# Performance work log

Measured on AMD Instinct MI355X. Metric: run time of the kernel, lower is better.

## Reference

```python
import jax, jax.numpy as jnp
import numpy as np

B, N, FD, HD, G = 32, 512, 768, 384, 3
ALPHA = 0.2  # LeakyReLU slope
NEG = -9e15


def layer_norm(x, g, b, eps=1e-5):
    m = jnp.mean(x, axis=-1, keepdims=True)
    v = jnp.var(x, axis=-1, keepdims=True)
    return (x - m) / jnp.sqrt(v + eps) * g + b


def gat_layer(x, adj, W, a):
    # x: [B,N,FD], adj: [N,N], W: [FD,HD], a: [2*HD]
    h = jnp.einsum('bnf,fd->bnd', x, W)  # [B,N,HD]
    # concat score decomposes: e_ij = lrelu(h_i . a[:HD] + h_j . a[HD:])
    e1 = h @ a[:HD]   # [B,N]
    e2 = h @ a[HD:]   # [B,N]
    e = jax.nn.leaky_relu(e1[:, :, None] + e2[:, None, :], ALPHA)  # [B,N,N]
    e = jnp.where(adj[None] > 0, e, NEG)
    att = jax.nn.softmax(e, axis=2)  # masked softmax over neighbors
    h_prime = jnp.einsum('bij,bjd->bid', att, h)
    return jax.nn.elu(h_prime)  # concat=True -> ELU


def setup_inputs() -> dict:
    key = jax.random.key(0)
    ks = jax.random.split(key, 10)
    s = 0.05
    return {
        'x': jax.random.normal(ks[0], (B, N, FD), jnp.float32),
        'adj': jax.random.randint(ks[1], (G, N, N), 0, 2),
        'W': jax.random.normal(ks[2], (G, FD, HD), jnp.float32) * s,
        'a': jax.random.normal(ks[3], (G, 2 * HD), jnp.float32) * s,
        'log_unc': jnp.zeros((G,), jnp.float32),
        'gate_w': jax.random.normal(ks[4], (FD, G), jnp.float32) * s,
        'gate_b': jnp.zeros((G,), jnp.float32),
        'ln1_g': jnp.ones((HD,), jnp.float32),
        'ln1_b': jnp.zeros((HD,), jnp.float32),
        'w1': jax.random.normal(ks[5], (HD, HD), jnp.float32) * s,
        'b1': jnp.zeros((HD,), jnp.float32),
        'w2': jax.random.normal(ks[6], (HD, FD), jnp.float32) * s,
        'b2': jnp.zeros((FD,), jnp.float32),
        'ln2_g': jnp.ones((FD,), jnp.float32),
        'ln2_b': jnp.zeros((FD,), jnp.float32),
    }


def reference(x, adj, W, a, log_unc, gate_w, gate_b, ln1_g, ln1_b,
              w1, b1, w2, b2, ln2_g, ln2_b):
    # global (uncertainty) weights
    unc = jnp.exp(log_unc)
    attw = jax.nn.softmax(1.0 / (unc + 1e-8))  # [G]
    # content gates from batch-averaged features
    avg = jnp.mean(x, axis=0)                          # [N,FD]
    cg = jax.nn.softmax(avg @ gate_w + gate_b, axis=-1)  # [N,G]
    # per-graph GAT + LayerNorm, vmapped over the G graphs
    gouts = jax.vmap(lambda ad, Wi, ai: layer_norm(gat_layer(x, ad, Wi, ai), ln1_g, ln1_b))(adj, W, a)  # [G,B,N,HD]
    weights = 0.7 * attw[:, None, None, None] + 0.3 * cg.T[:, None, :, None]  # [G,1|B,N,1]
    fused = jnp.sum(weights * gouts, axis=0)  # [B,N,HD]
    # output projection + LayerNorm
    proj = jax.nn.relu(fused @ w1 + b1) @ w2 + b2
    proj = layer_norm(proj, ln2_g, ln2_b)
    # residual gate
    gv = jax.nn.sigmoid(jnp.sum(proj * x, axis=-1, keepdims=True) / np.sqrt(FD).astype(np.float32))
    return gv * x + (1.0 - gv) * proj
```

## Files before the change

kernel.cpp:

```cpp
#include <hip/hip_runtime.h>

typedef unsigned short ushort_t;
typedef unsigned int uint_t;
typedef __bf16 bf16x8 __attribute__((ext_vector_type(8)));
typedef float f32x4 __attribute__((ext_vector_type(4)));
typedef unsigned int u32x4 __attribute__((ext_vector_type(4)));
typedef unsigned short u16x4 __attribute__((ext_vector_type(4)));
typedef unsigned short u16x8 __attribute__((ext_vector_type(8)));

#define B_SZ 32
#define N_SZ 512
#define FD_SZ 768
#define HD_SZ 384
#define G_SZ 3
#define M_SZ (B_SZ * N_SZ)
#define ALPHA_LR 0.2f
#define NEGV -9.0e15f
#define VTILE (HD_SZ * 32)
#define PSLICE ((size_t)M_SZ * HD_SZ)

__device__ __forceinline__ float bf2f(ushort_t u) { return __uint_as_float(((uint_t)u) << 16); }
__device__ __forceinline__ ushort_t f2bf(float f) {
  uint_t x = __float_as_uint(f);
  return (ushort_t)((x + 0x7fffu + ((x >> 16) & 1u)) >> 16);
}

__device__ __forceinline__ void gload_lds16(const ushort_t* g, ushort_t* l) {
  __builtin_amdgcn_global_load_lds(
      (const __attribute__((address_space(1))) uint_t*)(const void*)g,
      (__attribute__((address_space(3))) uint_t*)(void*)l, 16, 0, 0);
}

__global__ __launch_bounds__(256) void transpose_f2b(
    const float* __restrict__ src, ushort_t* __restrict__ dst, int R, int C) {
  size_t total = (size_t)R * C;
  size_t base = (size_t)blockIdx.z * total;
  size_t i = (size_t)blockIdx.x * 256 + threadIdx.x;
  if (i < total) {
    int r = (int)(i / C), c = (int)(i % C);
    dst[base + (size_t)c * R + r] = f2bf(src[base + i]);
  }
}

__global__ __launch_bounds__(256) void cast_f2b(
    const float* __restrict__ src, ushort_t* __restrict__ dst) {
  size_t i = (size_t)blockIdx.x * 256 + threadIdx.x;
  f32x4 v = ((const f32x4*)src)[i];
  u16x4 p;
  p[0] = f2bf(v.x); p[1] = f2bf(v.y); p[2] = f2bf(v.z); p[3] = f2bf(v.w);
  ((u16x4*)dst)[i] = p;
}

__global__ __launch_bounds__(256) void pack_adj(
    const int* __restrict__ adj, uint_t* __restrict__ am) {
  size_t i = (size_t)blockIdx.x * 256 + threadIdx.x;
  unsigned long long mask = __ballot(adj[i] != 0);
  int lane = threadIdx.x & 63;
  if ((lane & 31) == 0) am[i >> 5] = (uint_t)(mask >> (lane & 32));
}

__global__ __launch_bounds__(256) void gate_kernel(
    const float* __restrict__ x, const float* __restrict__ gate_w,
    const float* __restrict__ gate_b, float* __restrict__ cg) {
  int n = blockIdx.x;
  int tid = threadIdx.x;
  float a0 = 0.f, a1 = 0.f, a2 = 0.f;
  for (int f = tid; f < FD_SZ; f += 256) {
    float s = 0.f;
#pragma unroll
    for (int b = 0; b < B_SZ; b++) s += x[((size_t)b * N_SZ + n) * FD_SZ + f];
    float avg = s * (1.0f / B_SZ);
    a0 += avg * gate_w[f * 3 + 0];
    a1 += avg * gate_w[f * 3 + 1];
    a2 += avg * gate_w[f * 3 + 2];
  }
  for (int m = 1; m < 64; m <<= 1) {
    a0 += __shfl_xor(a0, m, 64);
    a1 += __shfl_xor(a1, m, 64);
    a2 += __shfl_xor(a2, m, 64);
  }
  __shared__ float red[3][4];
  int wave = tid >> 6, lane = tid & 63;
  if (lane == 0) { red[0][wave] = a0; red[1][wave] = a1; red[2][wave] = a2; }
  __syncthreads();
  if (tid == 0) {
    float l0 = red[0][0] + red[0][1] + red[0][2] + red[0][3] + gate_b[0];
    float l1 = red[1][0] + red[1][1] + red[1][2] + red[1][3] + gate_b[1];
    float l2 = red[2][0] + red[2][1] + red[2][2] + red[2][3] + gate_b[2];
    float mx = fmaxf(l0, fmaxf(l1, l2));
    float e0 = __expf(l0 - mx), e1 = __expf(l1 - mx), e2 = __expf(l2 - mx);
    float inv = 1.0f / (e0 + e1 + e2);
    cg[n * 3 + 0] = e0 * inv;
    cg[n * 3 + 1] = e1 * inv;
    cg[n * 3 + 2] = e2 * inv;
  }
}

template <bool RELU, bool OUTBF16, bool HASBIAS, bool VFOUT>
__global__ __launch_bounds__(256) void gemm_kernel(
    const ushort_t* __restrict__ Ab, size_t strideA,
    const ushort_t* __restrict__ Bt, size_t strideB,
    const float* __restrict__ bias,
    void* __restrict__ Cv, size_t strideC,
    int M, int K, int Nc) {
  __shared__ __attribute__((aligned(16))) ushort_t As[128 * 32];
  __shared__ __attribute__((aligned(16))) ushort_t Bs[128 * 32];
  int tid = threadIdx.x, wave = tid >> 6, lane = tid & 63;
  int m0 = blockIdx.y * 128, n0 = blockIdx.x * 128;
  const ushort_t* A = Ab + (size_t)blockIdx.z * strideA;
  const ushort_t* Bb = Bt + (size_t)blockIdx.z * strideB;

  f32x4 acc[4][4];
  f32x4 z4 = {0.f, 0.f, 0.f, 0.f};
#pragma unroll
  for (int i = 0; i < 4; i++)
#pragma unroll
    for (int j = 0; j < 4; j++) acc[i][j] = z4;

  int wm = (wave & 1) * 64, wn = (wave >> 1) * 64;
  int srow = lane >> 2, schk = (lane & 3) * 8;

  for (int kt = 0; kt < K; kt += 32) {
    __syncthreads();
#pragma unroll
    for (int i = 0; i < 2; i++) {
      int rowBase = wave * 32 + i * 16;
      gload_lds16(A + (size_t)(m0 + rowBase + srow) * K + kt + schk,
                  As + rowBase * 32);
      gload_lds16(Bb + (size_t)(n0 + rowBase + srow) * K + kt + schk,
                  Bs + rowBase * 32);
    }
    __syncthreads();
    bf16x8 af[4], bfr[4];
#pragma unroll
    for (int t = 0; t < 4; t++) {
      af[t] = *(const bf16x8*)(As + (wm + t * 16 + (lane & 15)) * 32 + (lane >> 4) * 8);
      bfr[t] = *(const bf16x8*)(Bs + (wn + t * 16 + (lane & 15)) * 32 + (lane >> 4) * 8);
    }
#pragma unroll
    for (int mt = 0; mt < 4; mt++)
#pragma unroll
      for (int nt = 0; nt < 4; nt++)
        acc[mt][nt] = __builtin_amdgcn_mfma_f32_16x16x32_bf16(af[mt], bfr[nt], acc[mt][nt], 0, 0, 0);
  }

  if (VFOUT) {
#pragma unroll
    for (int mt = 0; mt < 4; mt++) {
#pragma unroll
      for (int nt = 0; nt < 4; nt++) {
        int d = n0 + wn + nt * 16 + (lane & 15);
        int gm = m0 + wm + mt * 16 + (lane >> 4) * 4;
        int b = gm >> 9, jt = (gm >> 5) & 15, j2 = gm & 31;
        u16x4 pk;
#pragma unroll
        for (int r2 = 0; r2 < 4; r2++) pk[r2] = f2bf(acc[mt][nt][r2]);
        size_t off = ((size_t)((blockIdx.z * B_SZ + b) * 16 + jt)) * VTILE + (size_t)d * 32 + j2;
        *(u16x4*)((ushort_t*)Cv + off) = pk;
      }
    }
  } else {
#pragma unroll
    for (int mt = 0; mt < 4; mt++) {
#pragma unroll
      for (int nt = 0; nt < 4; nt++) {
        int gn = n0 + wn + nt * 16 + (lane & 15);
        float bvs = HASBIAS ? bias[gn] : 0.f;
#pragma unroll
        for (int r2 = 0; r2 < 4; r2++) {
          int gm = m0 + wm + mt * 16 + (lane >> 4) * 4 + r2;
          float v = acc[mt][nt][r2] + bvs;
          if (RELU) v = v > 0.f ? v : 0.f;
          size_t off = (size_t)blockIdx.z * strideC + (size_t)gm * Nc + gn;
          if (OUTBF16) ((ushort_t*)Cv)[off] = f2bf(v);
          else ((float*)Cv)[off] = v;
        }
      }
    }
  }
}

__global__ __launch_bounds__(256) void e12_kernel(
    const ushort_t* __restrict__ vf, const float* __restrict__ a,
    float* __restrict__ e1, float* __restrict__ e2) {
  __shared__ float a1s[HD_SZ], a2s[HD_SZ];
  int g = blockIdx.y;
  int tid = threadIdx.x;
  for (int i = tid; i < HD_SZ; i += 256) {
    a1s[i] = a[g * 2 * HD_SZ + i];
    a2s[i] = a[g * 2 * HD_SZ + HD_SZ + i];
  }
  __syncthreads();
  int m = blockIdx.x * 64 + (tid >> 2), dq = tid & 3;
  int b = m >> 9, jt = (m >> 5) & 15, j2 = m & 31;
  const ushort_t* col = vf + ((size_t)((g * B_SZ + b) * 16 + jt)) * VTILE + j2;
  float s1 = 0.f, s2 = 0.f;
#pragma unroll 4
  for (int k = 0; k < 96; k++) {
    int d = dq * 96 + k;
    float h = bf2f(col[d * 32]);
    s1 += h * a1s[d];
    s2 += h * a2s[d];
  }
  s1 += __shfl_xor(s1, 1, 64); s1 += __shfl_xor(s1, 2, 64);
  s2 += __shfl_xor(s2, 1, 64); s2 += __shfl_xor(s2, 2, 64);
  if (dq == 0) {
    e1[(size_t)g * M_SZ + m] = s1;
    e2[(size_t)g * M_SZ + m] = s2;
  }
}

__global__ __launch_bounds__(512, 4) void attn_kernel(
    const uint_t* __restrict__ adjm, const ushort_t* __restrict__ vf,
    const float* __restrict__ e1, const float* __restrict__ e2,
    const float* __restrict__ cg, const float* __restrict__ log_unc,
    const float* __restrict__ ln1g, const float* __restrict__ ln1b,
    ushort_t* __restrict__ pf) {
  __shared__ __attribute__((aligned(16))) ushort_t Pb[32][520];
  __shared__ float e2s[512];
  __shared__ float e1r[32];
  __shared__ uint_t amS[32][16];
  __shared__ float lng[HD_SZ], lnb[HD_SZ];
  __shared__ float cgr[32];
  __shared__ float s1s[32][8], s2s[32][8];

  int tid = threadIdx.x, wave = tid >> 6, lane = tid & 63;
  int quad = lane >> 4, l15 = lane & 15;
  int g = blockIdx.z;
  int L = blockIdx.x + (blockIdx.y << 4);
  int b = (L & 7) + ((L >> 7) << 3);
  int i0 = ((L >> 3) & 15) * 32;

  float iv0 = 1.f / (__expf(log_unc[0]) + 1e-8f);
  float iv1 = 1.f / (__expf(log_unc[1]) + 1e-8f);
  float iv2 = 1.f / (__expf(log_unc[2]) + 1e-8f);
  float mxa = fmaxf(iv0, fmaxf(iv1, iv2));
  float w0 = __expf(iv0 - mxa), w1 = __expf(iv1 - mxa), w2 = __expf(iv2 - mxa);
  float wsum = 1.f / (w0 + w1 + w2);
  float attwg = (g == 0 ? w0 : (g == 1 ? w1 : w2)) * wsum;

  if (tid < HD_SZ) {
    lng[tid] = ln1g[tid];
    lnb[tid] = ln1b[tid];
  }
  if (tid < 32) {
    cgr[tid] = cg[(i0 + tid) * 3 + g];
    e1r[tid] = e1[((size_t)g * B_SZ + b) * N_SZ + i0 + tid];
  }
  amS[tid >> 4][tid & 15] = adjm[((size_t)g * N_SZ + i0 + (tid >> 4)) * 16 + (tid & 15)];
  e2s[tid] = e2[((size_t)g * B_SZ + b) * N_SZ + tid];
  __syncthreads();

#pragma unroll
  for (int rr = 0; rr < 4; rr++) {
    int rw = wave * 4 + rr;
    float e1v = e1r[rw];
    float sv[8];
    float m = -3.0e38f;
#pragma unroll
    for (int jj = 0; jj < 8; jj++) {
      int j = lane + jj * 64;
      float s = e1v + e2s[j];
      s = s > 0.f ? s : ALPHA_LR * s;
      uint_t mw = amS[rw][(lane >> 5) + jj * 2];
      s = ((mw >> (j & 31)) & 1u) ? s : NEGV;
      sv[jj] = s;
      m = fmaxf(m, s);
    }
    for (int msk = 1; msk < 64; msk <<= 1) m = fmaxf(m, __shfl_xor(m, msk, 64));
    float sum = 0.f;
#pragma unroll
    for (int jj = 0; jj < 8; jj++) {
      float e = __expf(sv[jj] - m);
      sv[jj] = e;
      sum += e;
    }
    for (int msk = 1; msk < 64; msk <<= 1) sum += __shfl_xor(sum, msk, 64);
    float inv = 1.0f / sum;
#pragma unroll
    for (int jj = 0; jj < 8; jj++) Pb[rw][lane + jj * 64] = f2bf(sv[jj] * inv);
  }
  __syncthreads();

  f32x4 acc[2][3];
  f32x4 z4 = {0.f, 0.f, 0.f, 0.f};
#pragma unroll
  for (int mt = 0; mt < 2; mt++)
#pragma unroll
    for (int t = 0; t < 3; t++) acc[mt][t] = z4;
  const ushort_t* vbase = vf + ((size_t)(g * B_SZ + b) * 16) * VTILE;
  __builtin_amdgcn_s_setprio(1);
#pragma unroll 2
  for (int j0 = 0; j0 < N_SZ; j0 += 32) {
    const ushort_t* vtile = vbase + (size_t)(j0 >> 5) * VTILE;
    bf16x8 af0 = *(const bf16x8*)(&Pb[l15][j0 + quad * 8]);
    bf16x8 af1 = *(const bf16x8*)(&Pb[16 + l15][j0 + quad * 8]);
#pragma unroll
    for (int t = 0; t < 3; t++) {
      bf16x8 bf = *(const bf16x8*)(vtile + (wave * 48 + t * 16 + l15) * 32 + quad * 8);
      acc[0][t] = __builtin_amdgcn_mfma_f32_16x16x32_bf16(af0, bf, acc[0][t], 0, 0, 0);
      acc[1][t] = __builtin_amdgcn_mfma_f32_16x16x32_bf16(af1, bf, acc[1][t], 0, 0, 0);
    }
  }
  __builtin_amdgcn_s_setprio(0);

  float ps1[2][4], ps2[2][4];
#pragma unroll
  for (int mt = 0; mt < 2; mt++)
#pragma unroll
    for (int r = 0; r < 4; r++) { ps1[mt][r] = 0.f; ps2[mt][r] = 0.f; }
#pragma unroll
  for (int mt = 0; mt < 2; mt++)
#pragma unroll
    for (int t = 0; t < 3; t++)
#pragma unroll
      for (int r = 0; r < 4; r++) {
        float v = acc[mt][t][r];
        v = v > 0.f ? v : __expf(v) - 1.f;
        acc[mt][t][r] = v;
        ps1[mt][r] += v;
        ps2[mt][r] += v * v;
      }
#pragma unroll
  for (int msk = 1; msk < 16; msk <<= 1) {
#pragma unroll
    for (int mt = 0; mt < 2; mt++)
#pragma unroll
      for (int r = 0; r < 4; r++) {
        ps1[mt][r] += __shfl_xor(ps1[mt][r], msk, 64);
        ps2[mt][r] += __shfl_xor(ps2[mt][r], msk, 64);
      }
  }
  if (l15 == 0) {
#pragma unroll
    for (int mt = 0; mt < 2; mt++)
#pragma unroll
      for (int r = 0; r < 4; r++) {
        s1s[mt * 16 + quad * 4 + r][wave] = ps1[mt][r];
        s2s[mt * 16 + quad * 4 + r][wave] = ps2[mt][r];
      }
  }
  __syncthreads();
#pragma unroll
  for (int mt = 0; mt < 2; mt++)
#pragma unroll
    for (int r = 0; r < 4; r++) {
      int row = mt * 16 + quad * 4 + r;
      float S1 = 0.f, S2 = 0.f;
#pragma unroll
      for (int w = 0; w < 8; w++) {
        S1 += s1s[row][w];
        S2 += s2s[row][w];
      }
      float mean = S1 * (1.f / HD_SZ);
      float var = S2 * (1.f / HD_SZ) - mean * mean;
      float rs = rsqrtf(var + 1e-5f);
      float wgt = 0.7f * attwg + 0.3f * cgr[row];
      size_t rowo = (size_t)g * PSLICE + ((size_t)b * N_SZ + i0 + row) * HD_SZ;
#pragma unroll
      for (int t = 0; t < 3; t++) {
        int d = wave * 48 + t * 16 + l15;
        pf[rowo + d] = f2bf(wgt * ((acc[mt][t][r] - mean) * rs * lng[d] + lnb[d]));
      }
    }
}

__global__ __launch_bounds__(256) void reduce3_kernel(
    const ushort_t* __restrict__ pf, ushort_t* __restrict__ fused) {
  size_t u = ((size_t)blockIdx.x * 256 + threadIdx.x) * 8;
  u16x8 a = *(const u16x8*)(pf + u);
  u16x8 b = *(const u16x8*)(pf + PSLICE + u);
  u16x8 c = *(const u16x8*)(pf + 2 * PSLICE + u);
  u16x8 o;
#pragma unroll
  for (int k = 0; k < 8; k++)
    o[k] = f2bf(bf2f(a[k]) + bf2f(b[k]) + bf2f(c[k]));
  *(u16x8*)(fused + u) = o;
}

__global__ __launch_bounds__(256) void final_kernel(
    const ushort_t* __restrict__ projbf, const float* __restrict__ x,
    const float* __restrict__ ln2g, const float* __restrict__ ln2b,
    float* __restrict__ out) {
  int row = blockIdx.x;
  int tid = threadIdx.x, wave = tid >> 6, lane = tid & 63;
  const ushort_t* pr = projbf + (size_t)row * FD_SZ;
  const float* xr = x + (size_t)row * FD_SZ;
  float v[3], xv[3];
  float s1 = 0.f, s2 = 0.f;
#pragma unroll
  for (int k = 0; k < 3; k++) {
    int c = tid + k * 256;
    v[k] = bf2f(pr[c]);
    xv[k] = xr[c];
    s1 += v[k];
    s2 += v[k] * v[k];
  }
  for (int m = 1; m < 64; m <<= 1) {
    s1 += __shfl_xor(s1, m, 64);
    s2 += __shfl_xor(s2, m, 64);
  }
  __shared__ float rs1[4], rs2[4], rdt[4];
  if (lane == 0) { rs1[wave] = s1; rs2[wave] = s2; }
  __syncthreads();
  s1 = rs1[0] + rs1[1] + rs1[2] + rs1[3];
  s2 = rs2[0] + rs2[1] + rs2[2] + rs2[3];
  float mean = s1 * (1.f / FD_SZ);
  float var = s2 * (1.f / FD_SZ) - mean * mean;
  float rstd = rsqrtf(var + 1e-5f);
  float dot = 0.f;
  float pn[3];
#pragma unroll
  for (int k = 0; k < 3; k++) {
    int c = tid + k * 256;
    pn[k] = (v[k] - mean) * rstd * ln2g[c] + ln2b[c];
    dot += pn[k] * xv[k];
  }
  for (int m = 1; m < 64; m <<= 1) dot += __shfl_xor(dot, m, 64);
  if (lane == 0) rdt[wave] = dot;
  __syncthreads();
  dot = rdt[0] + rdt[1] + rdt[2] + rdt[3];
  float gv = 1.f / (1.f + __expf(-dot * (1.0f / 27.712812921102035f)));
#pragma unroll
  for (int k = 0; k < 3; k++) {
    int c = tid + k * 256;
    out[(size_t)row * FD_SZ + c] = gv * xv[k] + (1.f - gv) * pn[k];
  }
}

extern "C" void kernel_launch(void* const* d_in, const int* in_sizes, int n_in,
                              void* d_out, int out_size, void* d_ws, size_t ws_size,
                              hipStream_t stream) {
  (void)in_sizes; (void)n_in; (void)out_size; (void)ws_size;
  const float* x = (const float*)d_in[0];
  const int* adj = (const int*)d_in[1];
  const float* W = (const float*)d_in[2];
  const float* a = (const float*)d_in[3];
  const float* log_unc = (const float*)d_in[4];
  const float* gate_w = (const float*)d_in[5];
  const float* gate_b = (const float*)d_in[6];
  const float* ln1g = (const float*)d_in[7];
  const float* ln1b = (const float*)d_in[8];
  const float* w1 = (const float*)d_in[9];
  const float* b1 = (const float*)d_in[10];
  const float* w2 = (const float*)d_in[11];
  const float* b2 = (const float*)d_in[12];
  const float* ln2g = (const float*)d_in[13];
  const float* ln2b = (const float*)d_in[14];

  char* ws = (char*)d_ws;
  ushort_t* Wt      = (ushort_t*)(ws + 0);
  uint_t*   adjm    = (uint_t*)(ws + 0);
  ushort_t* w1t     = (ushort_t*)(ws + 1769472);
  ushort_t* w2t     = (ushort_t*)(ws + 2064384);
  float*    cg      = (float*)(ws + 2654208);
  float*    e1      = (float*)(ws + 2660352);
  float*    e2      = (float*)(ws + 2856960);
  ushort_t* fusedbf = (ushort_t*)(ws + 3053568);
  ushort_t* vf      = (ushort_t*)(ws + 15636480);
  ushort_t* t1bf    = (ushort_t*)(ws + 15636480);
  ushort_t* projbf  = (ushort_t*)(ws + 28219392);
  ushort_t* xb      = (ushort_t*)d_out;
  ushort_t* pf      = (ushort_t*)d_out;

  cast_f2b<<<dim3((M_SZ * FD_SZ) / 1024), 256, 0, stream>>>(x, xb);

  transpose_f2b<<<dim3(1152, 1, 3), 256, 0, stream>>>(W, Wt, FD_SZ, HD_SZ);
  transpose_f2b<<<dim3(576, 1, 1), 256, 0, stream>>>(w1, w1t, HD_SZ, HD_SZ);
  transpose_f2b<<<dim3(1152, 1, 1), 256, 0, stream>>>(w2, w2t, HD_SZ, FD_SZ);

  gate_kernel<<<dim3(N_SZ), 256, 0, stream>>>(x, gate_w, gate_b, cg);

  gemm_kernel<false, true, false, true><<<dim3(3, 128, 3), 256, 0, stream>>>(
      xb, 0, Wt, (size_t)HD_SZ * FD_SZ, nullptr, vf, 0,
      M_SZ, FD_SZ, HD_SZ);

  pack_adj<<<dim3((G_SZ * N_SZ * N_SZ) / 256), 256, 0, stream>>>(adj, adjm);

  e12_kernel<<<dim3(M_SZ / 64, G_SZ), 256, 0, stream>>>(vf, a, e1, e2);

  attn_kernel<<<dim3(N_SZ / 32, B_SZ, G_SZ), 512, 0, stream>>>(
      adjm, vf, e1, e2, cg, log_unc, ln1g, ln1b, pf);

  reduce3_kernel<<<dim3((M_SZ * HD_SZ) / (256 * 8)), 256, 0, stream>>>(pf, fusedbf);

  gemm_kernel<true, true, true, false><<<dim3(3, 128, 1), 256, 0, stream>>>(
      fusedbf, 0, w1t, 0, b1, t1bf, 0, M_SZ, HD_SZ, HD_SZ);
  gemm_kernel<false, true, true, false><<<dim3(6, 128, 1), 256, 0, stream>>>(
      t1bf, 0, w2t, 0, b2, projbf, 0, M_SZ, HD_SZ, FD_SZ);

  final_kernel<<<dim3(M_SZ), 256, 0, stream>>>(projbf, x, ln2g, ln2b, (float*)d_out);
}
```

Baseline: 335.9 us.

## Fuse cast into gate, e1/e2 into GEMM epilogue, reduce3 into W1 GEMM load

Several kernels are fused. The x-to-bf16 cast moves into the gate kernel, which already reads x. The e1/e2 attention projections are computed in the first GEMM epilogue with shuffles and atomics, replacing the separate e12 pass. The three-way graph reduction moves into the A-load of the first MLP GEMM. Weight transposes now use an LDS-tiled kernel, and the setprio hints are removed from the attention loop. This cuts launches and global round trips, at the cost of atomic float accumulation (order-dependent rounding), an extra zeroing kernel, and A-tile loads for the MLP GEMM that go through registers instead of direct-to-LDS.

```diff
diff --git a/kernel.cpp b/kernel.cpp
--- a/kernel.cpp
+++ b/kernel.cpp
@@ -31,24 +31,23 @@
       (__attribute__((address_space(3))) uint_t*)(void*)l, 16, 0, 0);
 }
 
-__global__ __launch_bounds__(256) void transpose_f2b(
+__global__ __launch_bounds__(256) void transpose_tile(
     const float* __restrict__ src, ushort_t* __restrict__ dst, int R, int C) {
-  size_t total = (size_t)R * C;
-  size_t base = (size_t)blockIdx.z * total;
-  size_t i = (size_t)blockIdx.x * 256 + threadIdx.x;
-  if (i < total) {
-    int r = (int)(i / C), c = (int)(i % C);
-    dst[base + (size_t)c * R + r] = f2bf(src[base + i]);
-  }
-}
-
-__global__ __launch_bounds__(256) void cast_f2b(
-    const float* __restrict__ src, ushort_t* __restrict__ dst) {
-  size_t i = (size_t)blockIdx.x * 256 + threadIdx.x;
-  f32x4 v = ((const f32x4*)src)[i];
-  u16x4 p;
-  p[0] = f2bf(v.x); p[1] = f2bf(v.y); p[2] = f2bf(v.z); p[3] = f2bf(v.w);
-  ((u16x4*)dst)[i] = p;
+  __shared__ float t[64][65];
+  size_t base = (size_t)blockIdx.z * R * C;
+  int c0 = blockIdx.x * 64, r0 = blockIdx.y * 64;
+  int tx = threadIdx.x & 63, ty = threadIdx.x >> 6;
+#pragma unroll
+  for (int i = 0; i < 16; i++) {
+    int r = ty * 16 + i;
+    t[r][tx] = src[base + (size_t)(r0 + r) * C + c0 + tx];
+  }
+  __syncthreads();
+#pragma unroll
+  for (int i = 0; i < 16; i++) {
+    int c = ty * 16 + i;
+    dst[base + (size_t)(c0 + c) * R + r0 + tx] = f2bf(t[tx][c]);
+  }
 }
 
 __global__ __launch_bounds__(256) void pack_adj(
@@ -59,16 +58,26 @@
   if ((lane & 31) == 0) am[i >> 5] = (uint_t)(mask >> (lane & 32));
 }
 
+__global__ __launch_bounds__(256) void zero_kernel(float* __restrict__ p) {
+  p[(size_t)blockIdx.x * 256 + threadIdx.x] = 0.f;
+}
+
 __global__ __launch_bounds__(256) void gate_kernel(
     const float* __restrict__ x, const float* __restrict__ gate_w,
-    const float* __restrict__ gate_b, float* __restrict__ cg) {
+    const float* __restrict__ gate_b, float* __restrict__ cg,
+    ushort_t* __restrict__ xb) {
   int n = blockIdx.x;
   int tid = threadIdx.x;
   float a0 = 0.f, a1 = 0.f, a2 = 0.f;
   for (int f = tid; f < FD_SZ; f += 256) {
     float s = 0.f;
 #pragma unroll
-    for (int b = 0; b < B_SZ; b++) s += x[((size_t)b * N_SZ + n) * FD_SZ + f];
+    for (int b = 0; b < B_SZ; b++) {
+      size_t off = ((size_t)b * N_SZ + n) * FD_SZ + f;
+      float xv = x[off];
+      xb[off] = f2bf(xv);
+      s += xv;
+    }
     float avg = s * (1.0f / B_SZ);
     a0 += avg * gate_w[f * 3 + 0];
     a1 += avg * gate_w[f * 3 + 1];
@@ -96,13 +105,15 @@
   }
 }
 
-template <bool RELU, bool OUTBF16, bool HASBIAS, bool VFOUT>
+template <bool RELU, bool OUTBF16, bool HASBIAS, bool VFOUT, bool EOUT, bool ARED3>
 __global__ __launch_bounds__(256) void gemm_kernel(
     const ushort_t* __restrict__ Ab, size_t strideA,
     const ushort_t* __restrict__ Bt, size_t strideB,
     const float* __restrict__ bias,
     void* __restrict__ Cv, size_t strideC,
-    int M, int K, int Nc) {
+    int M, int K, int Nc,
+    const float* __restrict__ av, float* __restrict__ e1,
+    float* __restrict__ e2) {
   __shared__ __attribute__((aligned(16))) ushort_t As[128 * 32];
   __shared__ __attribute__((aligned(16))) ushort_t Bs[128 * 32];
   int tid = threadIdx.x, wave = tid >> 6, lane = tid & 63;
@@ -121,12 +132,32 @@
   int srow = lane >> 2, schk = (lane & 3) * 8;
 
   for (int kt = 0; kt < K; kt += 32) {
+    u32x4 aw[2];
+    if (ARED3) {
+#pragma unroll
+      for (int i = 0; i < 2; i++) {
+        const ushort_t* ap =
+            A + (size_t)(m0 + wave * 32 + i * 16 + srow) * K + kt + schk;
+        u16x8 q0 = *(const u16x8*)ap;
+        u16x8 q1 = *(const u16x8*)(ap + PSLICE);
+        u16x8 q2 = *(const u16x8*)(ap + 2 * PSLICE);
+        union { ushort_t us[8]; u32x4 v; } pk;
+#pragma unroll
+        for (int k = 0; k < 8; k++)
+          pk.us[k] = f2bf(bf2f(q0[k]) + bf2f(q1[k]) + bf2f(q2[k]));
+        aw[i] = pk.v;
+      }
+    }
     __syncthreads();
 #pragma unroll
     for (int i = 0; i < 2; i++) {
       int rowBase = wave * 32 + i * 16;
-      gload_lds16(A + (size_t)(m0 + rowBase + srow) * K + kt + schk,
-                  As + rowBase * 32);
+      if (ARED3) {
+        *(u32x4*)(As + rowBase * 32 + lane * 8) = aw[i];
+      } else {
+        gload_lds16(A + (size_t)(m0 + rowBase + srow) * K + kt + schk,
+                    As + rowBase * 32);
+      }
       gload_lds16(Bb + (size_t)(n0 + rowBase + srow) * K + kt + schk,
                   Bs + rowBase * 32);
     }
@@ -158,6 +189,37 @@
         size_t off = ((size_t)((blockIdx.z * B_SZ + b) * 16 + jt)) * VTILE + (size_t)d * 32 + j2;
         *(u16x4*)((ushort_t*)Cv + off) = pk;
       }
+    }
+    if (EOUT) {
+      int g = blockIdx.z;
+      float a1v[4], a2v[4];
+#pragma unroll
+      for (int nt = 0; nt < 4; nt++) {
+        int d = n0 + wn + nt * 16 + (lane & 15);
+        a1v[nt] = av[g * 2 * HD_SZ + d];
+        a2v[nt] = av[g * 2 * HD_SZ + HD_SZ + d];
+      }
+#pragma unroll
+      for (int mt = 0; mt < 4; mt++)
+#pragma unroll
+        for (int r2 = 0; r2 < 4; r2++) {
+          float p1 = 0.f, p2 = 0.f;
+#pragma unroll
+          for (int nt = 0; nt < 4; nt++) {
+            p1 += acc[mt][nt][r2] * a1v[nt];
+            p2 += acc[mt][nt][r2] * a2v[nt];
+          }
+#pragma unroll
+          for (int msk = 1; msk < 16; msk <<= 1) {
+            p1 += __shfl_xor(p1, msk, 64);
+            p2 += __shfl_xor(p2, msk, 64);
+          }
+          if ((lane & 15) == 0) {
+            int gm = m0 + wm + mt * 16 + (lane >> 4) * 4 + r2;
+            atomicAdd(&e1[(size_t)g * M_SZ + gm], p1);
+            atomicAdd(&e2[(size_t)g * M_SZ + gm], p2);
+          }
+        }
     }
   } else {
 #pragma unroll
@@ -177,36 +239,6 @@
         }
       }
     }
-  }
-}
-
-__global__ __launch_bounds__(256) void e12_kernel(
-    const ushort_t* __restrict__ vf, const float* __restrict__ a,
-    float* __restrict__ e1, float* __restrict__ e2) {
-  __shared__ float a1s[HD_SZ], a2s[HD_SZ];
-  int g = blockIdx.y;
-  int tid = threadIdx.x;
-  for (int i = tid; i < HD_SZ; i += 256) {
-    a1s[i] = a[g * 2 * HD_SZ + i];
-    a2s[i] = a[g * 2 * HD_SZ + HD_SZ + i];
-  }
-  __syncthreads();
-  int m = blockIdx.x * 64 + (tid >> 2), dq = tid & 3;
-  int b = m >> 9, jt = (m >> 5) & 15, j2 = m & 31;
-  const ushort_t* col = vf + ((size_t)((g * B_SZ + b) * 16 + jt)) * VTILE + j2;
-  float s1 = 0.f, s2 = 0.f;
-#pragma unroll 4
-  for (int k = 0; k < 96; k++) {
-    int d = dq * 96 + k;
-    float h = bf2f(col[d * 32]);
-    s1 += h * a1s[d];
-    s2 += h * a2s[d];
-  }
-  s1 += __shfl_xor(s1, 1, 64); s1 += __shfl_xor(s1, 2, 64);
-  s2 += __shfl_xor(s2, 1, 64); s2 += __shfl_xor(s2, 2, 64);
-  if (dq == 0) {
-    e1[(size_t)g * M_SZ + m] = s1;
-    e2[(size_t)g * M_SZ + m] = s2;
   }
 }
 
@@ -289,7 +321,6 @@
 #pragma unroll
     for (int t = 0; t < 3; t++) acc[mt][t] = z4;
   const ushort_t* vbase = vf + ((size_t)(g * B_SZ + b) * 16) * VTILE;
-  __builtin_amdgcn_s_setprio(1);
 #pragma unroll 2
   for (int j0 = 0; j0 < N_SZ; j0 += 32) {
     const ushort_t* vtile = vbase + (size_t)(j0 >> 5) * VTILE;
@@ -302,7 +333,6 @@
       acc[1][t] = __builtin_amdgcn_mfma_f32_16x16x32_bf16(af1, bf, acc[1][t], 0, 0, 0);
     }
   }
-  __builtin_amdgcn_s_setprio(0);
 
   float ps1[2][4], ps2[2][4];
 #pragma unroll
@@ -363,19 +393,6 @@
         pf[rowo + d] = f2bf(wgt * ((acc[mt][t][r] - mean) * rs * lng[d] + lnb[d]));
       }
     }
-}
-
-__global__ __launch_bounds__(256) void reduce3_kernel(
-    const ushort_t* __restrict__ pf, ushort_t* __restrict__ fused) {
-  size_t u = ((size_t)blockIdx.x * 256 + threadIdx.x) * 8;
-  u16x8 a = *(const u16x8*)(pf + u);
-  u16x8 b = *(const u16x8*)(pf + PSLICE + u);
-  u16x8 c = *(const u16x8*)(pf + 2 * PSLICE + u);
-  u16x8 o;
-#pragma unroll
-  for (int k = 0; k < 8; k++)
-    o[k] = f2bf(bf2f(a[k]) + bf2f(b[k]) + bf2f(c[k]));
-  *(u16x8*)(fused + u) = o;
 }
 
 __global__ __launch_bounds__(256) void final_kernel(
@@ -456,38 +473,33 @@
   float*    cg      = (float*)(ws + 2654208);
   float*    e1      = (float*)(ws + 2660352);
   float*    e2      = (float*)(ws + 2856960);
-  ushort_t* fusedbf = (ushort_t*)(ws + 3053568);
   ushort_t* vf      = (ushort_t*)(ws + 15636480);
   ushort_t* t1bf    = (ushort_t*)(ws + 15636480);
   ushort_t* projbf  = (ushort_t*)(ws + 28219392);
   ushort_t* xb      = (ushort_t*)d_out;
   ushort_t* pf      = (ushort_t*)d_out;
 
-  cast_f2b<<<dim3((M_SZ * FD_SZ) / 1024), 256, 0, stream>>>(x, xb);
-
-  transpose_f2b<<<dim3(1152, 1, 3), 256, 0, stream>>>(W, Wt, FD_SZ, HD_SZ);
-  transpose_f2b<<<dim3(576, 1, 1), 256, 0, stream>>>(w1, w1t, HD_SZ, HD_SZ);
-  transpose_f2b<<<dim3(1152, 1, 1), 256, 0, stream>>>(w2, w2t, HD_SZ, FD_SZ);
-
-  gate_kernel<<<dim3(N_SZ), 256, 0, stream>>>(x, gate_w, gate_b, cg);
-
-  gemm_kernel<false, true, false, true><<<dim3(3, 128, 3), 256, 0, stream>>>(
+  transpose_tile<<<dim3(HD_SZ / 64, FD_SZ / 64, 3), 256, 0, stream>>>(W, Wt, FD_SZ, HD_SZ);
+  transpose_tile<<<dim3(HD_SZ / 64, HD_SZ / 64, 1), 256, 0, stream>>>(w1, w1t, HD_SZ, HD_SZ);
+  transpose_tile<<<dim3(FD_SZ / 64, HD_SZ / 64, 1), 256, 0, stream>>>(w2, w2t, HD_SZ, FD_SZ);
+
+  gate_kernel<<<dim3(N_SZ), 256, 0, stream>>>(x, gate_w, gate_b, cg, xb);
+
+  zero_kernel<<<dim3((2 * G_SZ * M_SZ) / 256), 256, 0, stream>>>(e1);
+
+  gemm_kernel<false, true, false, true, true, false><<<dim3(3, 128, 3), 256, 0, stream>>>(
       xb, 0, Wt, (size_t)HD_SZ * FD_SZ, nullptr, vf, 0,
-      M_SZ, FD_SZ, HD_SZ);
+      M_SZ, FD_SZ, HD_SZ, a, e1, e2);
 
   pack_adj<<<dim3((G_SZ * N_SZ * N_SZ) / 256), 256, 0, stream>>>(adj, adjm);
-
-  e12_kernel<<<dim3(M_SZ / 64, G_SZ), 256, 0, stream>>>(vf, a, e1, e2);
 
   attn_kernel<<<dim3(N_SZ / 32, B_SZ, G_SZ), 512, 0, stream>>>(
       adjm, vf, e1, e2, cg, log_unc, ln1g, ln1b, pf);
 
-  reduce3_kernel<<<dim3((M_SZ * HD_SZ) / (256 * 8)), 256, 0, stream>>>(pf, fusedbf);
-
-  gemm_kernel<true, true, true, false><<<dim3(3, 128, 1), 256, 0, stream>>>(
-      fusedbf, 0, w1t, 0, b1, t1bf, 0, M_SZ, HD_SZ, HD_SZ);
-  gemm_kernel<false, true, true, false><<<dim3(6, 128, 1), 256, 0, stream>>>(
-      t1bf, 0, w2t, 0, b2, projbf, 0, M_SZ, HD_SZ, FD_SZ);
+  gemm_kernel<true, true, true, false, false, true><<<dim3(3, 128, 1), 256, 0, stream>>>(
+      pf, 0, w1t, 0, b1, t1bf, 0, M_SZ, HD_SZ, HD_SZ, nullptr, nullptr, nullptr);
+  gemm_kernel<false, true, true, false, false, false><<<dim3(6, 128, 1), 256, 0, stream>>>(
+      t1bf, 0, w2t, 0, b2, projbf, 0, M_SZ, HD_SZ, FD_SZ, nullptr, nullptr, nullptr);
 
   final_kernel<<<dim3(M_SZ), 256, 0, stream>>>(projbf, x, ln2g, ln2b, (float*)d_out);
 }
```

New measurement: 327.6 us. 2.5% less time.
